# Kernel tuning notes

Hardware: AMD Instinct MI355X
Metric: run time of the kernel (lower is better)

## Reference

```python
import jax, jax.numpy as jnp
import numpy as np

# Module hyperparams (from init_kwargs)
VX, VY = 0.16, 0.16
PC_RANGE = (0.0, -39.68, -3.0, 69.12, 39.68, 1.0)
X_OFFSET = VX / 2 + PC_RANGE[0]
Y_OFFSET = VY / 2 + PC_RANGE[1]
X_L = int((PC_RANGE[3] - PC_RANGE[0]) / VX)  # 432
Y_L = int((PC_RANGE[4] - PC_RANGE[1]) / VY)  # 496
IN_CH, OUT_CH = 9, 64
BN_EPS = 1e-3
P, N_MAX, B = 40000, 32, 4


def setup_inputs() -> dict:
    key = jax.random.key(0)
    k1, k2, k3 = jax.random.split(key, 3)
    pillars = jax.random.normal(k1, (P, N_MAX, 4), dtype=jnp.float32)
    # Unique (per batch) pillar coordinates so the scatter is well-defined.
    rng = np.random.default_rng(0)
    per = P // B
    rows = []
    for b in range(B):
        lin = rng.choice(Y_L * X_L, size=per, replace=False)
        ys, xs = lin // X_L, lin % X_L
        rows.append(np.stack([np.full(per, b, np.int32), xs.astype(np.int32), ys.astype(np.int32)], axis=1))
    coors_batch = jnp.asarray(np.concatenate(rows, axis=0))  # (P,3): [b, x, y]
    npoints_per_pillar = jax.random.randint(k2, (P,), 1, N_MAX + 1, dtype=jnp.int32)
    # Learned params: 1x1 Conv1d weight (no bias) + BN affine
    W = jax.random.normal(k3, (OUT_CH, IN_CH), dtype=jnp.float32) * 0.1
    gamma = jnp.ones((OUT_CH,), dtype=jnp.float32)
    beta = jnp.zeros((OUT_CH,), dtype=jnp.float32)
    return {"pillars": pillars, "coors_batch": coors_batch,
            "npoints_per_pillar": npoints_per_pillar,
            "W": W, "gamma": gamma, "beta": beta, "batch_size": B}


def reference(pillars, coors_batch, npoints_per_pillar, W, gamma, beta, batch_size):
    npts = npoints_per_pillar.astype(pillars.dtype)
    # offset of each point from pillar mean (xyz)
    center = jnp.sum(pillars[:, :, :3], axis=1, keepdims=True) / npts[:, None, None]
    offset_pt_center = pillars[:, :, :3] - center                      # (P,N,3)
    cx = coors_batch[:, None, 1:2].astype(pillars.dtype) * VX + X_OFFSET
    cy = coors_batch[:, None, 2:3].astype(pillars.dtype) * VY + Y_OFFSET
    x_off = pillars[:, :, :1] - cx                                     # (P,N,1)
    y_off = pillars[:, :, 1:2] - cy                                    # (P,N,1)
    features = jnp.concatenate([pillars, offset_pt_center, x_off, y_off], axis=-1)  # (P,N,9)
    mask = (jnp.arange(N_MAX)[None, :] < npoints_per_pillar[:, None]).astype(features.dtype)
    features = features * mask[:, :, None]
    # 1x1 Conv1d == per-point channel mix -> (P, C_out, N)
    x = jnp.einsum('pnc,oc->pon', features, W)
    # BatchNorm1d (training-mode stats over pillar and point dims, biased var)
    mean = jnp.mean(x, axis=(0, 2))
    var = jnp.var(x, axis=(0, 2))
    x = gamma[None, :, None] * (x - mean[None, :, None]) * jax.lax.rsqrt(var[None, :, None] + BN_EPS) + beta[None, :, None]
    x = jax.nn.relu(x)
    pooled = jnp.max(x, axis=-1)                                       # (P, C_out)
    # Single vectorized scatter into BEV canvas: (B, Y, X, C) then -> (B, C, Y, X)
    canvas = jnp.zeros((batch_size, Y_L, X_L, OUT_CH), dtype=jnp.float32)
    canvas = canvas.at[coors_batch[:, 0], coors_batch[:, 2], coors_batch[:, 1]].set(pooled)
    return jnp.transpose(canvas, (0, 3, 1, 2))
```

## Files before the change

### kernel.cpp

```cpp
#include <hip/hip_runtime.h>
#include <math.h>

#define P_TOT 40000
#define NMAX 32
#define BATCH 4
#define YL 496
#define XL 432
#define CIN 9
#define COUT 64
#define NTRI 45
#define PN_F 1280000.0f

#define MAP_ELEMS (BATCH * YL * XL)
#define MAP_BYTES (MAP_ELEMS * 4)
#define STATS_OFF MAP_BYTES
#define SCALE_OFF (STATS_OFF + 256)
#define SHIFT_OFF (SCALE_OFF + 256)
#define POOLED_OFF (SHIFT_OFF + 256)

#define STATS_BLOCKS 256

__global__ __launch_bounds__(256) void k_init(int* __restrict__ map,
                                              float* __restrict__ stats) {
    int i = blockIdx.x * 256 + threadIdx.x;
    if (i < MAP_ELEMS) map[i] = -1;
    if (i < 54) stats[i] = 0.0f;
}

__global__ __launch_bounds__(256) void k_stats(const float4* __restrict__ pillars,
                                               const int* __restrict__ coors,
                                               const int* __restrict__ npp,
                                               int* __restrict__ map,
                                               float* __restrict__ stats) {
    const int wave = threadIdx.x >> 6;
    const int lane = threadIdx.x & 63;
    const int half = lane >> 5;
    const int n = lane & 31;
    const int gw = blockIdx.x * 4 + wave;
    const int totalWaves = STATS_BLOCKS * 4;

    float s1[CIN];
    float s2[NTRI];
#pragma unroll
    for (int i = 0; i < CIN; i++) s1[i] = 0.0f;
#pragma unroll
    for (int i = 0; i < NTRI; i++) s2[i] = 0.0f;

    for (int p0 = gw * 2; p0 < P_TOT; p0 += totalWaves * 2) {
        int p = p0 + half;
        float4 q = pillars[(size_t)p * NMAX + n];

        float sx = q.x, sy = q.y, sz = q.z;
#pragma unroll
        for (int off = 1; off < 32; off <<= 1) {
            sx += __shfl_xor(sx, off, 32);
            sy += __shfl_xor(sy, off, 32);
            sz += __shfl_xor(sz, off, 32);
        }
        int npts = npp[p];
        float fn = (float)npts;
        float mx = sx / fn, my = sy / fn, mz = sz / fn;

        int xi = coors[p * 3 + 1];
        int yi = coors[p * 3 + 2];
        if (n == 0) {
            int b = coors[p * 3 + 0];
            map[(b * YL + yi) * XL + xi] = p;
        }
        float cx = (float)xi * 0.16f + 0.08f;
        float cy = (float)yi * 0.16f + (-39.6f);

        float msk = (n < npts) ? 1.0f : 0.0f;
        float f[CIN];
        f[0] = q.x * msk; f[1] = q.y * msk; f[2] = q.z * msk; f[3] = q.w * msk;
        f[4] = (q.x - mx) * msk; f[5] = (q.y - my) * msk; f[6] = (q.z - mz) * msk;
        f[7] = (q.x - cx) * msk; f[8] = (q.y - cy) * msk;

        int k = 0;
#pragma unroll
        for (int a = 0; a < CIN; a++) {
            s1[a] += f[a];
#pragma unroll
            for (int c = a; c < CIN; c++) s2[k++] += f[a] * f[c];
        }
    }

#pragma unroll
    for (int i = 0; i < CIN; i++) {
        float v = s1[i];
        for (int off = 1; off < 64; off <<= 1) v += __shfl_xor(v, off, 64);
        s1[i] = v;
    }
#pragma unroll
    for (int i = 0; i < NTRI; i++) {
        float v = s2[i];
        for (int off = 1; off < 64; off <<= 1) v += __shfl_xor(v, off, 64);
        s2[i] = v;
    }

    __shared__ float red[4][54];
    if (lane == 0) {
#pragma unroll
        for (int i = 0; i < CIN; i++) red[wave][i] = s1[i];
#pragma unroll
        for (int i = 0; i < NTRI; i++) red[wave][CIN + i] = s2[i];
    }
    __syncthreads();
    if (threadIdx.x < 54) {
        float v = red[0][threadIdx.x] + red[1][threadIdx.x] +
                  red[2][threadIdx.x] + red[3][threadIdx.x];
        atomicAdd(&stats[threadIdx.x], v);
    }
}

__global__ void k_finalize(const float* __restrict__ W,
                           const float* __restrict__ gamma,
                           const float* __restrict__ beta,
                           const float* __restrict__ stats,
                           float* __restrict__ scale,
                           float* __restrict__ shift) {
    int o = threadIdx.x;
    float w[CIN];
#pragma unroll
    for (int c = 0; c < CIN; c++) w[c] = W[o * CIN + c];

    const float invPN = 1.0f / PN_F;
    float mu = 0.0f;
#pragma unroll
    for (int c = 0; c < CIN; c++) mu += w[c] * (stats[c] * invPN);

    float ex2 = 0.0f;
    int k = 0;
#pragma unroll
    for (int a = 0; a < CIN; a++) {
#pragma unroll
        for (int c = a; c < CIN; c++) {
            float Mv = stats[CIN + k] * invPN;
            float t = w[a] * w[c] * Mv;
            ex2 += (a == c) ? t : 2.0f * t;
            k++;
        }
    }
    float var = ex2 - mu * mu;
    float sc = gamma[o] * rsqrtf(var + 1e-3f);
    scale[o] = sc;
    shift[o] = beta[o] - mu * sc;
}

__global__ __launch_bounds__(256) void k_pool(const float4* __restrict__ pillars,
                                              const int* __restrict__ coors,
                                              const int* __restrict__ npp,
                                              const float* __restrict__ W,
                                              const float* __restrict__ scale,
                                              const float* __restrict__ shift,
                                              float* __restrict__ pooled) {
    __shared__ float fsh[4][NMAX][CIN];
    int w = threadIdx.x >> 6;
    int lane = threadIdx.x & 63;
    int p = blockIdx.x * 4 + w;
    int n = lane & 31;

    float4 q = pillars[(size_t)p * NMAX + n];
    float sx = q.x, sy = q.y, sz = q.z;
#pragma unroll
    for (int off = 1; off < 32; off <<= 1) {
        sx += __shfl_xor(sx, off, 32);
        sy += __shfl_xor(sy, off, 32);
        sz += __shfl_xor(sz, off, 32);
    }
    int npts = npp[p];
    float fn = (float)npts;
    float mx = sx / fn, my = sy / fn, mz = sz / fn;
    int xi = coors[p * 3 + 1];
    int yi = coors[p * 3 + 2];
    float cx = (float)xi * 0.16f + 0.08f;
    float cy = (float)yi * 0.16f + (-39.6f);

    if (lane < 32) {
        bool valid = (n < npts);
        fsh[w][n][0] = valid ? q.x : 0.0f;
        fsh[w][n][1] = valid ? q.y : 0.0f;
        fsh[w][n][2] = valid ? q.z : 0.0f;
        fsh[w][n][3] = valid ? q.w : 0.0f;
        fsh[w][n][4] = valid ? (q.x - mx) : 0.0f;
        fsh[w][n][5] = valid ? (q.y - my) : 0.0f;
        fsh[w][n][6] = valid ? (q.z - mz) : 0.0f;
        fsh[w][n][7] = valid ? (q.x - cx) : 0.0f;
        fsh[w][n][8] = valid ? (q.y - cy) : 0.0f;
    }
    __syncthreads();

    float wv[CIN];
#pragma unroll
    for (int c = 0; c < CIN; c++) wv[c] = W[lane * CIN + c];
    float sc = scale[lane];
    float sh = shift[lane];

    float m = -INFINITY;
#pragma unroll 4
    for (int nn = 0; nn < NMAX; nn++) {
        float d = 0.0f;
#pragma unroll
        for (int c = 0; c < CIN; c++) d += wv[c] * fsh[w][nn][c];
        m = fmaxf(m, sc * d + sh);
    }
    pooled[(size_t)p * COUT + lane] = fmaxf(m, 0.0f);
}

__global__ __launch_bounds__(256) void k_scatter(const int* __restrict__ map,
                                                 const float* __restrict__ pooled,
                                                 float* __restrict__ out) {
    int i = blockIdx.x * 256 + threadIdx.x;
    if (i >= BATCH * YL * (XL / 4)) return;
    int x4 = i % (XL / 4);
    int r = i / (XL / 4);
    int y = r % YL;
    int b = r / YL;

    const int4 pid = *(const int4*)(map + (size_t)(b * YL + y) * XL + x4 * 4);
    size_t obase = ((size_t)(b * COUT) * YL + y) * XL + (size_t)x4 * 4;
    const size_t cstride = (size_t)YL * XL;

    const float4 zero = make_float4(0.f, 0.f, 0.f, 0.f);
#pragma unroll 4
    for (int c4 = 0; c4 < COUT / 4; c4++) {
        float4 r0 = zero, r1 = zero, r2 = zero, r3 = zero;
        if (pid.x >= 0) r0 = *(const float4*)(pooled + (size_t)pid.x * COUT + c4 * 4);
        if (pid.y >= 0) r1 = *(const float4*)(pooled + (size_t)pid.y * COUT + c4 * 4);
        if (pid.z >= 0) r2 = *(const float4*)(pooled + (size_t)pid.z * COUT + c4 * 4);
        if (pid.w >= 0) r3 = *(const float4*)(pooled + (size_t)pid.w * COUT + c4 * 4);
        float* o0 = out + obase + (size_t)(c4 * 4) * cstride;
        *(float4*)(o0)               = make_float4(r0.x, r1.x, r2.x, r3.x);
        *(float4*)(o0 + cstride)     = make_float4(r0.y, r1.y, r2.y, r3.y);
        *(float4*)(o0 + 2 * cstride) = make_float4(r0.z, r1.z, r2.z, r3.z);
        *(float4*)(o0 + 3 * cstride) = make_float4(r0.w, r1.w, r2.w, r3.w);
    }
}

extern "C" void kernel_launch(void* const* d_in, const int* in_sizes, int n_in,
                              void* d_out, int out_size, void* d_ws, size_t ws_size,
                              hipStream_t stream) {
    const float4* pillars = (const float4*)d_in[0];
    const int* coors = (const int*)d_in[1];
    const int* npp = (const int*)d_in[2];
    const float* W = (const float*)d_in[3];
    const float* gamma = (const float*)d_in[4];
    const float* beta = (const float*)d_in[5];
    float* out = (float*)d_out;

    char* ws = (char*)d_ws;
    int* map = (int*)(ws);
    float* stats = (float*)(ws + STATS_OFF);
    float* scale = (float*)(ws + SCALE_OFF);
    float* shift = (float*)(ws + SHIFT_OFF);
    float* pooled = (float*)(ws + POOLED_OFF);

    k_init<<<(MAP_ELEMS + 255) / 256, 256, 0, stream>>>(map, stats);
    k_stats<<<STATS_BLOCKS, 256, 0, stream>>>(pillars, coors, npp, map, stats);
    k_finalize<<<1, 64, 0, stream>>>(W, gamma, beta, stats, scale, shift);
    k_pool<<<P_TOT / 4, 256, 0, stream>>>(pillars, coors, npp, W, scale, shift, pooled);
    k_scatter<<<(BATCH * YL * (XL / 4) + 255) / 256, 256, 0, stream>>>(map, pooled, out);
}
```

Measured before the change: 315.2 us.

## Fold BN scale and per-pillar offsets into weights, pool via lane broadcasts

The finalize kernel now folds the BN scale into the conv weights and precombines the channels that depend on x, y and z, so each output channel needs only a 4-term dot product plus a per-pillar bias. The pool kernel drops its shared-memory feature staging and block barrier, reads points with readlane broadcasts, and loops only over valid points. Masked points are handled by seeding the max with the shift value. Stats blocks also go from 256 to 512. The per-pillar loop becomes scalar-uniform, and there is a small floating-point reassociation difference.

```diff
diff --git a/kernel.cpp b/kernel.cpp
--- a/kernel.cpp
+++ b/kernel.cpp
@@ -14,11 +14,10 @@
 #define MAP_ELEMS (BATCH * YL * XL)
 #define MAP_BYTES (MAP_ELEMS * 4)
 #define STATS_OFF MAP_BYTES
-#define SCALE_OFF (STATS_OFF + 256)
-#define SHIFT_OFF (SCALE_OFF + 256)
-#define POOLED_OFF (SHIFT_OFF + 256)
-
-#define STATS_BLOCKS 256
+#define CONSTS_OFF (STATS_OFF + 256)
+#define POOLED_OFF (CONSTS_OFF + 4096)
+
+#define STATS_BLOCKS 512
 
 __global__ __launch_bounds__(256) void k_init(int* __restrict__ map,
                                               float* __restrict__ stats) {
@@ -117,8 +116,7 @@
                            const float* __restrict__ gamma,
                            const float* __restrict__ beta,
                            const float* __restrict__ stats,
-                           float* __restrict__ scale,
-                           float* __restrict__ shift) {
+                           float* __restrict__ consts) {
     int o = threadIdx.x;
     float w[CIN];
 #pragma unroll
@@ -143,18 +141,28 @@
     }
     float var = ex2 - mu * mu;
     float sc = gamma[o] * rsqrtf(var + 1e-3f);
-    scale[o] = sc;
-    shift[o] = beta[o] - mu * sc;
+    float sh = beta[o] - mu * sc;
+
+    float* cc = consts + o * 12;
+    cc[0] = sc * (w[0] + w[4] + w[7]);
+    cc[1] = sc * (w[1] + w[5] + w[8]);
+    cc[2] = sc * (w[2] + w[6]);
+    cc[3] = sc * w[3];
+    cc[4] = sc * w[4];
+    cc[5] = sc * w[5];
+    cc[6] = sc * w[6];
+    cc[7] = sc * w[7];
+    cc[8] = sc * w[8];
+    cc[9] = sh;
+    cc[10] = 0.0f;
+    cc[11] = 0.0f;
 }
 
 __global__ __launch_bounds__(256) void k_pool(const float4* __restrict__ pillars,
                                               const int* __restrict__ coors,
                                               const int* __restrict__ npp,
-                                              const float* __restrict__ W,
-                                              const float* __restrict__ scale,
-                                              const float* __restrict__ shift,
+                                              const float* __restrict__ consts,
                                               float* __restrict__ pooled) {
-    __shared__ float fsh[4][NMAX][CIN];
     int w = threadIdx.x >> 6;
     int lane = threadIdx.x & 63;
     int p = blockIdx.x * 4 + w;
@@ -168,7 +176,7 @@
         sy += __shfl_xor(sy, off, 32);
         sz += __shfl_xor(sz, off, 32);
     }
-    int npts = npp[p];
+    int npts = __builtin_amdgcn_readfirstlane(npp[p]);
     float fn = (float)npts;
     float mx = sx / fn, my = sy / fn, mz = sz / fn;
     int xi = coors[p * 3 + 1];
@@ -176,33 +184,20 @@
     float cx = (float)xi * 0.16f + 0.08f;
     float cy = (float)yi * 0.16f + (-39.6f);
 
-    if (lane < 32) {
-        bool valid = (n < npts);
-        fsh[w][n][0] = valid ? q.x : 0.0f;
-        fsh[w][n][1] = valid ? q.y : 0.0f;
-        fsh[w][n][2] = valid ? q.z : 0.0f;
-        fsh[w][n][3] = valid ? q.w : 0.0f;
-        fsh[w][n][4] = valid ? (q.x - mx) : 0.0f;
-        fsh[w][n][5] = valid ? (q.y - my) : 0.0f;
-        fsh[w][n][6] = valid ? (q.z - mz) : 0.0f;
-        fsh[w][n][7] = valid ? (q.x - cx) : 0.0f;
-        fsh[w][n][8] = valid ? (q.y - cy) : 0.0f;
-    }
-    __syncthreads();
-
-    float wv[CIN];
-#pragma unroll
-    for (int c = 0; c < CIN; c++) wv[c] = W[lane * CIN + c];
-    float sc = scale[lane];
-    float sh = shift[lane];
-
-    float m = -INFINITY;
-#pragma unroll 4
-    for (int nn = 0; nn < NMAX; nn++) {
-        float d = 0.0f;
-#pragma unroll
-        for (int c = 0; c < CIN; c++) d += wv[c] * fsh[w][nn][c];
-        m = fmaxf(m, sc * d + sh);
+    const float4* cc = (const float4*)consts + lane * 3;
+    float4 c0 = cc[0];
+    float4 c1 = cc[1];
+    float4 c2 = cc[2];
+    float B = c2.y - (c1.x * mx + c1.y * my + c1.z * mz + c1.w * cx + c2.x * cy);
+
+    float m = (npts < NMAX) ? c2.y : -INFINITY;
+    for (int j = 0; j < npts; ++j) {
+        float qx = __uint_as_float(__builtin_amdgcn_readlane(__float_as_uint(q.x), j));
+        float qy = __uint_as_float(__builtin_amdgcn_readlane(__float_as_uint(q.y), j));
+        float qz = __uint_as_float(__builtin_amdgcn_readlane(__float_as_uint(q.z), j));
+        float qw = __uint_as_float(__builtin_amdgcn_readlane(__float_as_uint(q.w), j));
+        float d = fmaf(c0.x, qx, fmaf(c0.y, qy, fmaf(c0.z, qz, fmaf(c0.w, qw, B))));
+        m = fmaxf(m, d);
     }
     pooled[(size_t)p * COUT + lane] = fmaxf(m, 0.0f);
 }
@@ -251,13 +246,12 @@
     char* ws = (char*)d_ws;
     int* map = (int*)(ws);
     float* stats = (float*)(ws + STATS_OFF);
-    float* scale = (float*)(ws + SCALE_OFF);
-    float* shift = (float*)(ws + SHIFT_OFF);
+    float* consts = (float*)(ws + CONSTS_OFF);
     float* pooled = (float*)(ws + POOLED_OFF);
 
     k_init<<<(MAP_ELEMS + 255) / 256, 256, 0, stream>>>(map, stats);
     k_stats<<<STATS_BLOCKS, 256, 0, stream>>>(pillars, coors, npp, map, stats);
-    k_finalize<<<1, 64, 0, stream>>>(W, gamma, beta, stats, scale, shift);
-    k_pool<<<P_TOT / 4, 256, 0, stream>>>(pillars, coors, npp, W, scale, shift, pooled);
+    k_finalize<<<1, 64, 0, stream>>>(W, gamma, beta, stats, consts);
+    k_pool<<<P_TOT / 4, 256, 0, stream>>>(pillars, coors, npp, consts, pooled);
     k_scatter<<<(BATCH * YL * (XL / 4) + 255) / 256, 256, 0, stream>>>(map, pooled, out);
 }
```

Result: faster. 289.9 us (-8.0%).
